# Kernel tuning notes

Measured on AMD Instinct MI355X. Metric: run time of the kernel, lower is better.

## Reference

```python
import jax, jax.numpy as jnp
import numpy as np

B, C, G, P = 4, 64, 64, 8  # batch, in_dims, grid_size, patch_size


def setup_inputs() -> dict:
    key = jax.random.key(0)
    k1, k2 = jax.random.split(key)
    fea = jax.random.normal(k1, (B, G * G, C), dtype=jnp.float32)
    prob = jax.random.uniform(k2, (B, 9, G * P, G * P), dtype=jnp.float32)
    return {"fea": fea, "prob": prob}


def reference(fea, prob):
    # fea: [B, G*G, C] -> kv: [B, C, G, G]
    kv = fea.transpose(0, 2, 1).reshape(B, C, G, G)
    # replicate pad by 1 on each spatial side
    kv_pad = jnp.pad(kv, ((0, 0), (0, 0), (1, 1), (1, 1)), mode="edge")
    # 9 shifted 3x3-neighbor views (row-major dy,dx order matches kv1..kv9;
    # center view kv_pad[:,:,1:-1,1:-1] == kv exactly under replicate pad)
    shifts = [kv_pad[:, :, dy:dy + G, dx:dx + G]
              for dy in range(3) for dx in range(3)]
    kv_merge = jnp.stack(shifts, axis=1)                      # [B,9,C,G,G]
    kv_merge = kv_merge.reshape(B, 9, C, G * G).transpose(0, 3, 1, 2)  # [B,G^2,9,C]
    # prob: [B,9,G*P,G*P] -> attn: [B, G^2, P^2, 9]  (local_arrange)
    attn = (prob.reshape(B, 9, G, P, G, P)
                .transpose(0, 2, 4, 3, 5, 1)
                .reshape(B, G * G, P * P, 9))
    # attention-weighted sum over the 9 neighbors
    out = jnp.einsum("bnpk,bnkc->bnpc", attn, kv_merge)      # [B,G^2,P^2,C]
    # local_rearrange: [B,(h w),(p1 p2),c] -> [B,c,(h p1),(w p2)]
    out = (out.reshape(B, G, G, P, P, C)
              .transpose(0, 5, 1, 3, 2, 4)
              .reshape(B, C, G * P, G * P))
    return out
```

## Files before the change

kernel.cpp:

```cpp
#include <hip/hip_runtime.h>

constexpr int Bn = 4;
constexpr int Cn = 64;
constexpr int Gn = 64;
constexpr int Pn = 8;
constexpr int Sn = Gn * Pn;

constexpr int CPB   = 16;
constexpr int XSPAN = CPB * Pn;
constexpr int NXB   = Sn / XSPAN;
constexpr int COLS  = CPB + 2;
constexpr int LDC   = 68;

__global__ __launch_bounds__(256, 2)
void sp_upsample_kernel(const float* __restrict__ fea,
                        const float* __restrict__ prob,
                        float* __restrict__ out) {
    __shared__ float fea_lds[3 * COLS * LDC];

    const int bx  = blockIdx.x;
    const int xb  = bx & (NXB - 1);
    const int h   = (bx >> 2) & (Gn - 1);
    const int b   = bx >> 8;
    const int w0  = xb * CPB;
    const int x0  = xb * XSPAN;
    const int tid = threadIdx.x;

    constexpr int NVEC = 3 * COLS * (Cn / 4);
    for (int idx = tid; idx < NVEC; idx += 256) {
        const int c4   = idx & 15;
        const int colr = idx >> 4;
        const int col  = colr % COLS;
        const int r    = colr / COLS;
        const int gh = min(max(h - 1 + r, 0), Gn - 1);
        const int gw = min(max(w0 - 1 + col, 0), Gn - 1);
        const float4 v = *reinterpret_cast<const float4*>(
            fea + ((size_t)(b * Gn * Gn + gh * Gn + gw)) * Cn + c4 * 4);
        *reinterpret_cast<float4*>(&fea_lds[(r * COLS + col) * LDC + c4 * 4]) = v;
    }
    __syncthreads();

    const int xl   = tid & (XSPAN - 1);
    const int p1q  = tid >> 7;
    const int x    = x0 + xl;
    const int cell = xl >> 3;
    const int ybase = h * Pn + p1q * 4;

    float p[4][9];
    const size_t SS = (size_t)Sn * Sn;
    #pragma unroll
    for (int r = 0; r < 4; ++r) {
        const float* pb = prob + (size_t)b * 9 * SS + (size_t)(ybase + r) * Sn + x;
        #pragma unroll
        for (int k = 0; k < 9; ++k)
            p[r][k] = __builtin_nontemporal_load(pb + (size_t)k * SS);
    }

    float* ob = out + (size_t)b * Cn * SS;

    #pragma unroll 1
    for (int c4 = 0; c4 < Cn / 4; ++c4) {
        float4 f[9];
        #pragma unroll
        for (int k = 0; k < 9; ++k) {
            const int dy = k / 3, dx = k % 3;
            f[k] = *reinterpret_cast<const float4*>(
                &fea_lds[(dy * COLS + cell + dx) * LDC + c4 * 4]);
        }
        float4 acc[4];
        #pragma unroll
        for (int r = 0; r < 4; ++r) acc[r] = make_float4(0.f, 0.f, 0.f, 0.f);
        #pragma unroll
        for (int k = 0; k < 9; ++k) {
            #pragma unroll
            for (int r = 0; r < 4; ++r) {
                acc[r].x = fmaf(p[r][k], f[k].x, acc[r].x);
                acc[r].y = fmaf(p[r][k], f[k].y, acc[r].y);
                acc[r].z = fmaf(p[r][k], f[k].z, acc[r].z);
                acc[r].w = fmaf(p[r][k], f[k].w, acc[r].w);
            }
        }
        #pragma unroll
        for (int r = 0; r < 4; ++r) {
            const size_t base = (size_t)(c4 * 4) * SS + (size_t)(ybase + r) * Sn + x;
            __builtin_nontemporal_store(acc[r].x, ob + base);
            __builtin_nontemporal_store(acc[r].y, ob + base + SS);
            __builtin_nontemporal_store(acc[r].z, ob + base + 2 * SS);
            __builtin_nontemporal_store(acc[r].w, ob + base + 3 * SS);
        }
    }
}

extern "C" void kernel_launch(void* const* d_in, const int* in_sizes, int n_in,
                              void* d_out, int out_size, void* d_ws, size_t ws_size,
                              hipStream_t stream) {
    const float* fea  = (const float*)d_in[0];
    const float* prob = (const float*)d_in[1];
    float* out = (float*)d_out;

    const int grid = Bn * Gn * NXB;
    sp_upsample_kernel<<<grid, 256, 0, stream>>>(fea, prob, out);
}
```

Measured before the change: 62.72 us.

## Process two column tiles per block and prefetch second tile's prob via LDS DMA

Each block now covers two adjacent 16-cell column tiles, which halves the grid and widens the shared feature halo. The second tile's attention weights are loaded asynchronously into LDS with global_load_lds while the first tile is computed, then read from LDS for the second tile. The intent is to hide prob load latency behind the output-store loop and share the feature halo load. The cost is more LDS per block and less block-level parallelism. It also depends on the DMA writes to LDS being complete before the barrier.

```diff
diff --git a/kernel.cpp b/kernel.cpp
--- a/kernel.cpp
+++ b/kernel.cpp
@@ -1,4 +1,5 @@
 #include <hip/hip_runtime.h>
+#include <stdint.h>
 
 constexpr int Bn = 4;
 constexpr int Cn = 64;
@@ -8,68 +9,29 @@
 
 constexpr int CPB   = 16;
 constexpr int XSPAN = CPB * Pn;
-constexpr int NXB   = Sn / XSPAN;
-constexpr int COLS  = CPB + 2;
+constexpr int PAIRW = 2 * CPB;
+constexpr int COLS  = PAIRW + 2;
 constexpr int LDC   = 68;
 
-__global__ __launch_bounds__(256, 2)
-void sp_upsample_kernel(const float* __restrict__ fea,
-                        const float* __restrict__ prob,
-                        float* __restrict__ out) {
-    __shared__ float fea_lds[3 * COLS * LDC];
+typedef float f32x4 __attribute__((ext_vector_type(4)));
+typedef const __attribute__((address_space(1))) uint32_t gu32;
+typedef __attribute__((address_space(3)))       uint32_t lu32;
 
-    const int bx  = blockIdx.x;
-    const int xb  = bx & (NXB - 1);
-    const int h   = (bx >> 2) & (Gn - 1);
-    const int b   = bx >> 8;
-    const int w0  = xb * CPB;
-    const int x0  = xb * XSPAN;
-    const int tid = threadIdx.x;
-
-    constexpr int NVEC = 3 * COLS * (Cn / 4);
-    for (int idx = tid; idx < NVEC; idx += 256) {
-        const int c4   = idx & 15;
-        const int colr = idx >> 4;
-        const int col  = colr % COLS;
-        const int r    = colr / COLS;
-        const int gh = min(max(h - 1 + r, 0), Gn - 1);
-        const int gw = min(max(w0 - 1 + col, 0), Gn - 1);
-        const float4 v = *reinterpret_cast<const float4*>(
-            fea + ((size_t)(b * Gn * Gn + gh * Gn + gw)) * Cn + c4 * 4);
-        *reinterpret_cast<float4*>(&fea_lds[(r * COLS + col) * LDC + c4 * 4]) = v;
-    }
-    __syncthreads();
-
-    const int xl   = tid & (XSPAN - 1);
-    const int p1q  = tid >> 7;
-    const int x    = x0 + xl;
-    const int cell = xl >> 3;
-    const int ybase = h * Pn + p1q * 4;
-
-    float p[4][9];
-    const size_t SS = (size_t)Sn * Sn;
-    #pragma unroll
-    for (int r = 0; r < 4; ++r) {
-        const float* pb = prob + (size_t)b * 9 * SS + (size_t)(ybase + r) * Sn + x;
-        #pragma unroll
-        for (int k = 0; k < 9; ++k)
-            p[r][k] = __builtin_nontemporal_load(pb + (size_t)k * SS);
-    }
-
-    float* ob = out + (size_t)b * Cn * SS;
-
+__device__ __forceinline__ void tile_compute(const float* fea_lds,
+                                             const float (&p)[4][9],
+                                             int cell, float* obase, size_t SS) {
     #pragma unroll 1
     for (int c4 = 0; c4 < Cn / 4; ++c4) {
-        float4 f[9];
+        f32x4 f[9];
         #pragma unroll
         for (int k = 0; k < 9; ++k) {
             const int dy = k / 3, dx = k % 3;
-            f[k] = *reinterpret_cast<const float4*>(
+            f[k] = *reinterpret_cast<const f32x4*>(
                 &fea_lds[(dy * COLS + cell + dx) * LDC + c4 * 4]);
         }
-        float4 acc[4];
+        f32x4 acc[4];
         #pragma unroll
-        for (int r = 0; r < 4; ++r) acc[r] = make_float4(0.f, 0.f, 0.f, 0.f);
+        for (int r = 0; r < 4; ++r) acc[r] = (f32x4)(0.f);
         #pragma unroll
         for (int k = 0; k < 9; ++k) {
             #pragma unroll
@@ -82,13 +44,92 @@
         }
         #pragma unroll
         for (int r = 0; r < 4; ++r) {
-            const size_t base = (size_t)(c4 * 4) * SS + (size_t)(ybase + r) * Sn + x;
-            __builtin_nontemporal_store(acc[r].x, ob + base);
-            __builtin_nontemporal_store(acc[r].y, ob + base + SS);
-            __builtin_nontemporal_store(acc[r].z, ob + base + 2 * SS);
-            __builtin_nontemporal_store(acc[r].w, ob + base + 3 * SS);
+            const size_t base = (size_t)(c4 * 4) * SS + (size_t)r * Sn;
+            __builtin_nontemporal_store(acc[r].x, obase + base);
+            __builtin_nontemporal_store(acc[r].y, obase + base + SS);
+            __builtin_nontemporal_store(acc[r].z, obase + base + 2 * SS);
+            __builtin_nontemporal_store(acc[r].w, obase + base + 3 * SS);
         }
     }
+}
+
+__global__ __launch_bounds__(256, 2)
+void sp_upsample_kernel(const float* __restrict__ fea,
+                        const float* __restrict__ prob,
+                        float* __restrict__ out) {
+    __shared__ float fea_lds[3 * COLS * LDC];
+    __shared__ float p_lds[9][Pn][XSPAN];
+
+    const int bx  = blockIdx.x;
+    const int pr  = bx & 1;
+    const int h   = (bx >> 1) & (Gn - 1);
+    const int b   = bx >> 7;
+    const int w0  = pr * PAIRW;
+    const int tid = threadIdx.x;
+    const size_t SS = (size_t)Sn * Sn;
+
+    constexpr int NVEC = 3 * COLS * (Cn / 4);
+    for (int idx = tid; idx < NVEC; idx += 256) {
+        const int c4   = idx & 15;
+        const int colr = idx >> 4;
+        const int col  = colr % COLS;
+        const int r    = colr / COLS;
+        const int gh = min(max(h - 1 + r, 0), Gn - 1);
+        const int gw = min(max(w0 - 1 + col, 0), Gn - 1);
+        const f32x4 v = *reinterpret_cast<const f32x4*>(
+            fea + ((size_t)(b * Gn * Gn + gh * Gn + gw)) * Cn + c4 * 4);
+        *reinterpret_cast<f32x4*>(&fea_lds[(r * COLS + col) * LDC + c4 * 4]) = v;
+    }
+    __syncthreads();
+
+    const int xl    = tid & (XSPAN - 1);
+    const int p1q   = tid >> 7;
+    const int ybase = h * Pn + p1q * 4;
+    const int lane  = tid & 63;
+    const int wv    = tid >> 6;
+    const int x0    = pr * 256 + xl;
+
+    float p0[4][9];
+    {
+        const float* pb = prob + (size_t)b * 9 * SS + (size_t)ybase * Sn + x0;
+        #pragma unroll
+        for (int r = 0; r < 4; ++r)
+            #pragma unroll
+            for (int k = 0; k < 9; ++k)
+                p0[r][k] = __builtin_nontemporal_load(pb + (size_t)r * Sn + (size_t)k * SS);
+    }
+    __builtin_amdgcn_sched_barrier(0);
+
+    {
+        const float* pbase = prob + (size_t)b * 9 * SS;
+        const int x01 = pr * 256 + XSPAN;
+        for (int j = wv; j < 144; j += 4) {
+            const int k    = j >> 4;
+            const int rem  = j & 15;
+            const int y    = rem >> 1;
+            const int half = rem & 1;
+            const float* g = pbase + (size_t)k * SS + (size_t)(h * Pn + y) * Sn
+                             + x01 + half * 64 + lane;
+            __builtin_amdgcn_global_load_lds((gu32*)g, (lu32*)&p_lds[k][y][half * 64],
+                                             4, 0, 0);
+        }
+    }
+    __builtin_amdgcn_sched_barrier(0);
+
+    float* ob0 = out + (size_t)b * Cn * SS + (size_t)ybase * Sn + x0;
+    tile_compute(fea_lds, p0, (xl >> 3), ob0, SS);
+
+    __syncthreads();
+
+    float p1[4][9];
+    #pragma unroll
+    for (int r = 0; r < 4; ++r)
+        #pragma unroll
+        for (int k = 0; k < 9; ++k)
+            p1[r][k] = p_lds[k][p1q * 4 + r][xl];
+
+    float* ob1 = ob0 + XSPAN;
+    tile_compute(fea_lds, p1, CPB + (xl >> 3), ob1, SS);
 }
 
 extern "C" void kernel_launch(void* const* d_in, const int* in_sizes, int n_in,
@@ -98,6 +139,6 @@
     const float* prob = (const float*)d_in[1];
     float* out = (float*)d_out;
 
-    const int grid = Bn * Gn * NXB;
+    const int grid = Bn * Gn * 2;
     sp_upsample_kernel<<<grid, 256, 0, stream>>>(fea, prob, out);
 }
```

New measurement: 63.87 us. About the same (+1.8%).
